# Performance work log

Measured on AMD Instinct MI355X. Metric: run time of the kernel, lower is better.

The kernel has to match this reference:

```python
import jax, jax.numpy as jnp
import numpy as np

EMBED_DIM = 512
NUM_HEADS = 8
DPH = EMBED_DIM // NUM_HEADS
NUM_REL = 3
B, S = 8, 512


def setup_inputs() -> dict:
    key = jax.random.key(0)
    ks = jax.random.split(key, 12)
    sc = 1.0 / np.sqrt(EMBED_DIM)
    inp = {
        'query': jax.random.normal(ks[0], (B, S, EMBED_DIM), jnp.float32),
        'key': jax.random.normal(ks[1], (B, S, EMBED_DIM), jnp.float32),
        'value': jax.random.normal(ks[2], (B, S, EMBED_DIM), jnp.float32),
        'graph_relations': jax.random.randint(ks[3], (B, S, S), 0, NUM_REL, jnp.int32),
        'Wq': jax.random.normal(ks[4], (EMBED_DIM, EMBED_DIM), jnp.float32) * sc,
        'bq': jnp.zeros((EMBED_DIM,), jnp.float32),
        'Wk': jax.random.normal(ks[5], (EMBED_DIM, EMBED_DIM), jnp.float32) * sc,
        'bk': jnp.zeros((EMBED_DIM,), jnp.float32),
        'Wv': jax.random.normal(ks[6], (EMBED_DIM, EMBED_DIM), jnp.float32) * sc,
        'bv': jnp.zeros((EMBED_DIM,), jnp.float32),
        'Wo': jax.random.normal(ks[7], (EMBED_DIM, EMBED_DIM), jnp.float32) * sc,
        'bo': jnp.zeros((EMBED_DIM,), jnp.float32),
        # padding_idx=0 -> row 0 is zeros
        'rel_k': jax.random.normal(ks[8], (NUM_REL, DPH), jnp.float32).at[0].set(0.0),
        'rel_v': jax.random.normal(ks[9], (NUM_REL, DPH), jnp.float32).at[0].set(0.0),
    }
    return inp


def reference(query, key, value, graph_relations, Wq, bq, Wk, bk, Wv, bv, Wo, bo, rel_k, rel_v):
    scale = DPH ** (-0.5)
    b, s, _ = query.shape
    # projections + split into heads: [b, s, h, d]
    q = (query @ Wq + bq).reshape(b, s, NUM_HEADS, DPH)
    k = (key @ Wk + bk).reshape(b, s, NUM_HEADS, DPH)
    v = (value @ Wv + bv).reshape(b, s, NUM_HEADS, DPH)
    QK = jnp.einsum('bshd,bthd->bhst', q, k)
    E_k = rel_k[graph_relations]  # [b, s, t, d]
    QE = jnp.einsum('bshd,bstd->bhst', q, E_k)
    e = jax.nn.softmax((QK + QE) * scale, axis=-1)  # [b, h, s, t]
    eV = jnp.einsum('bhst,bthd->bshd', e, v)
    E_v = rel_v[graph_relations]  # [b, s, t, d]
    eE = jnp.einsum('bhst,bstd->bshd', e, E_v)
    out = (eV + eE).reshape(b, s, EMBED_DIM)
    return out @ Wo + bo
```

## Files before the change

### kernel.cpp

```cpp
#include <hip/hip_runtime.h>
#include <hip/hip_bf16.h>

#define S_LEN 512
#define EMB   512
#define NHEAD 8
#define DPH   64
#define NREL  3
#define BATCH 8

typedef __attribute__((ext_vector_type(8))) short bf16x8;
typedef __attribute__((ext_vector_type(4))) float f32x4;

__device__ __forceinline__ float bf2f(unsigned short u) {
    union { unsigned int i; float f; } cv;
    cv.i = ((unsigned int)u) << 16;
    return cv.f;
}
__device__ __forceinline__ unsigned short f2bf(float f) {
    __hip_bfloat16 h = __float2bfloat16(f);
    return *reinterpret_cast<unsigned short*>(&h);
}

__device__ __forceinline__ void gload_lds16(const unsigned short* g, unsigned char* lds) {
    __builtin_amdgcn_global_load_lds(
        (const __attribute__((address_space(1))) void*)g,
        (__attribute__((address_space(3))) void*)lds, 16, 0, 0);
}

__global__ __launch_bounds__(256) void transpose_w(
    const float* __restrict__ Wq, const float* __restrict__ Wk,
    const float* __restrict__ Wv, const float* __restrict__ Wo,
    unsigned short* __restrict__ Wt)
{
    const int z = blockIdx.z;
    const float* W = (z == 0) ? Wq : (z == 1) ? Wk : (z == 2) ? Wv : Wo;
    unsigned short* dst = Wt + (size_t)z * EMB * EMB;

    __shared__ float tile[64][65];
    const int n0 = blockIdx.x * 64, k0 = blockIdx.y * 64;
    const int t = threadIdx.x;
    const int cr = t >> 4, cc = (t & 15) * 4;

    #pragma unroll
    for (int it = 0; it < 4; ++it) {
        int r = cr + it * 16;
        float4 v = *reinterpret_cast<const float4*>(W + (size_t)(k0 + r) * EMB + n0 + cc);
        tile[r][cc + 0] = v.x; tile[r][cc + 1] = v.y;
        tile[r][cc + 2] = v.z; tile[r][cc + 3] = v.w;
    }
    __syncthreads();
    #pragma unroll
    for (int it = 0; it < 4; ++it) {
        int n = cr + it * 16;
        ushort4 o;
        o.x = f2bf(tile[cc + 0][n]); o.y = f2bf(tile[cc + 1][n]);
        o.z = f2bf(tile[cc + 2][n]); o.w = f2bf(tile[cc + 3][n]);
        *reinterpret_cast<ushort4*>(dst + (size_t)(n0 + n) * EMB + k0 + cc) = o;
    }
}

__global__ __launch_bounds__(256) void gemm_proj_mfma(
    const float* __restrict__ Aq, const float* __restrict__ Ak, const float* __restrict__ Av,
    const unsigned short* __restrict__ Wt,
    const float* __restrict__ bqp, const float* __restrict__ bkp, const float* __restrict__ bvp,
    unsigned short* __restrict__ oq, unsigned short* __restrict__ okp, unsigned short* __restrict__ ov)
{
    const int z = blockIdx.z;
    const float* A = (z == 0) ? Aq : (z == 1) ? Ak : Av;
    const unsigned short* W = Wt + (size_t)z * EMB * EMB;
    const float* bias = (z == 0) ? bqp : (z == 1) ? bkp : bvp;
    unsigned short* out = (z == 0) ? oq : (z == 1) ? okp : ov;

    const int n0 = blockIdx.x * 128;
    const int m0 = blockIdx.y * 64;
    const int tid = threadIdx.x;
    const int lane = tid & 63;
    const int wid = tid >> 6;
    const int wr = wid >> 1, wc = wid & 1;

    __shared__ __align__(16) unsigned char smA[64 * 64 * 2];
    __shared__ __align__(16) unsigned char smB[128 * 64 * 2];

    f32x4 acc[2][4] = {};

    for (int k0 = 0; k0 < EMB; k0 += 64) {
        __syncthreads();
        #pragma unroll
        for (int it = 0; it < 4; ++it) {
            int row = (it * 4 + wid) * 8 + (lane >> 3);
            int kcg = (lane & 7) ^ (row & 7);
            gload_lds16(W + (size_t)(n0 + row) * EMB + k0 + kcg * 8,
                        smB + (it * 4 + wid) * 1024);
        }
        #pragma unroll
        for (int it = 0; it < 2; ++it) {
            int w = it * 256 + tid;
            int row = w >> 3, kc = w & 7;
            const float* src = A + (size_t)(m0 + row) * EMB + k0 + kc * 8;
            float4 v0 = *reinterpret_cast<const float4*>(src);
            float4 v1 = *reinterpret_cast<const float4*>(src + 4);
            union { unsigned short s[8]; uint4 u; } p;
            p.s[0] = f2bf(v0.x); p.s[1] = f2bf(v0.y); p.s[2] = f2bf(v0.z); p.s[3] = f2bf(v0.w);
            p.s[4] = f2bf(v1.x); p.s[5] = f2bf(v1.y); p.s[6] = f2bf(v1.z); p.s[7] = f2bf(v1.w);
            unsigned byte = ((unsigned)row << 7) + ((unsigned)kc << 4);
            byte ^= (unsigned)((row & 7) << 4);
            *reinterpret_cast<uint4*>(smA + byte) = p.u;
        }
        __syncthreads();

        #pragma unroll
        for (int ks = 0; ks < 2; ++ks) {
            bf16x8 bfrag[4];
            #pragma unroll
            for (int ni = 0; ni < 4; ++ni) {
                int col = wc * 64 + ni * 16 + (lane & 15);
                unsigned byte = ((unsigned)col << 7) + (unsigned)(ks << 6) + (unsigned)((lane >> 4) << 4);
                byte ^= (unsigned)((col & 7) << 4);
                bfrag[ni] = *reinterpret_cast<const bf16x8*>(smB + byte);
            }
            #pragma unroll
            for (int mi = 0; mi < 2; ++mi) {
                int row = wr * 32 + mi * 16 + (lane & 15);
                unsigned byte = ((unsigned)row << 7) + (unsigned)(ks << 6) + (unsigned)((lane >> 4) << 4);
                byte ^= (unsigned)((row & 7) << 4);
                bf16x8 afrag = *reinterpret_cast<const bf16x8*>(smA + byte);
                #pragma unroll
                for (int ni = 0; ni < 4; ++ni)
                    acc[mi][ni] = __builtin_amdgcn_mfma_f32_16x16x32_bf16(afrag, bfrag[ni], acc[mi][ni], 0, 0, 0);
            }
        }
    }

    if (z == 2) {
        #pragma unroll
        for (int ni = 0; ni < 4; ++ni) {
            int colg = n0 + wc * 64 + ni * 16 + (lane & 15);
            float bj = bias[colg];
            int hh = colg >> 6, dd = colg & 63;
            #pragma unroll
            for (int mi = 0; mi < 2; ++mi) {
                int rbase = m0 + wr * 32 + mi * 16 + ((lane >> 4) << 2);
                int bb = rbase >> 9, ss = rbase & 511;
                ushort4 o;
                o.x = f2bf(acc[mi][ni][0] + bj);
                o.y = f2bf(acc[mi][ni][1] + bj);
                o.z = f2bf(acc[mi][ni][2] + bj);
                o.w = f2bf(acc[mi][ni][3] + bj);
                *reinterpret_cast<ushort4*>(out + ((size_t)(bb * NHEAD + hh) * DPH + dd) * S_LEN + ss) = o;
            }
        }
    } else {
        #pragma unroll
        for (int ni = 0; ni < 4; ++ni) {
            int colg = n0 + wc * 64 + ni * 16 + (lane & 15);
            float bj = bias[colg];
            #pragma unroll
            for (int mi = 0; mi < 2; ++mi) {
                int rbase = m0 + wr * 32 + mi * 16 + ((lane >> 4) << 2);
                #pragma unroll
                for (int q = 0; q < 4; ++q)
                    out[(size_t)(rbase + q) * EMB + colg] = f2bf(acc[mi][ni][q] + bj);
            }
        }
    }
}

__global__ __launch_bounds__(256) void gemm_out_mfma(
    const unsigned short* __restrict__ A,
    const unsigned short* __restrict__ W,
    const float* __restrict__ bias,
    float* __restrict__ out)
{
    const int n0 = blockIdx.x * 128;
    const int m0 = blockIdx.y * 64;
    const int tid = threadIdx.x;
    const int lane = tid & 63;
    const int wid = tid >> 6;
    const int wr = wid >> 1, wc = wid & 1;

    __shared__ __align__(16) unsigned char smA[64 * 64 * 2];
    __shared__ __align__(16) unsigned char smB[128 * 64 * 2];

    f32x4 acc[2][4] = {};

    for (int k0 = 0; k0 < EMB; k0 += 64) {
        __syncthreads();
        #pragma unroll
        for (int it = 0; it < 4; ++it) {
            int row = (it * 4 + wid) * 8 + (lane >> 3);
            int kcg = (lane & 7) ^ (row & 7);
            gload_lds16(W + (size_t)(n0 + row) * EMB + k0 + kcg * 8,
                        smB + (it * 4 + wid) * 1024);
        }
        #pragma unroll
        for (int it = 0; it < 2; ++it) {
            int row = (it * 4 + wid) * 8 + (lane >> 3);
            int kcg = (lane & 7) ^ (row & 7);
            gload_lds16(A + (size_t)(m0 + row) * EMB + k0 + kcg * 8,
                        smA + (it * 4 + wid) * 1024);
        }
        __syncthreads();

        #pragma unroll
        for (int ks = 0; ks < 2; ++ks) {
            bf16x8 bfrag[4];
            #pragma unroll
            for (int ni = 0; ni < 4; ++ni) {
                int col = wc * 64 + ni * 16 + (lane & 15);
                unsigned byte = ((unsigned)col << 7) + (unsigned)(ks << 6) + (unsigned)((lane >> 4) << 4);
                byte ^= (unsigned)((col & 7) << 4);
                bfrag[ni] = *reinterpret_cast<const bf16x8*>(smB + byte);
            }
            #pragma unroll
            for (int mi = 0; mi < 2; ++mi) {
                int row = wr * 32 + mi * 16 + (lane & 15);
                unsigned byte = ((unsigned)row << 7) + (unsigned)(ks << 6) + (unsigned)((lane >> 4) << 4);
                byte ^= (unsigned)((row & 7) << 4);
                bf16x8 afrag = *reinterpret_cast<const bf16x8*>(smA + byte);
                #pragma unroll
                for (int ni = 0; ni < 4; ++ni)
                    acc[mi][ni] = __builtin_amdgcn_mfma_f32_16x16x32_bf16(afrag, bfrag[ni], acc[mi][ni], 0, 0, 0);
            }
        }
    }

    #pragma unroll
    for (int ni = 0; ni < 4; ++ni) {
        int colg = n0 + wc * 64 + ni * 16 + (lane & 15);
        float bj = bias[colg];
        #pragma unroll
        for (int mi = 0; mi < 2; ++mi) {
            int rbase = m0 + wr * 32 + mi * 16 + ((lane >> 4) << 2);
            #pragma unroll
            for (int q = 0; q < 4; ++q)
                out[(size_t)(rbase + q) * EMB + colg] = acc[mi][ni][q] + bj;
        }
    }
}

__global__ __launch_bounds__(512) void attn_mfma(
    const unsigned short* __restrict__ qb,
    const unsigned short* __restrict__ kb,
    const unsigned short* __restrict__ vbT,
    const int* __restrict__ rel,
    const float* __restrict__ rel_k, const float* __restrict__ rel_v,
    unsigned short* __restrict__ ob)
{
    const int gid = blockIdx.x + 8 * (blockIdx.y + 8 * blockIdx.z);
    const int bh  = (gid & 7) + 8 * ((gid >> 3) & 7);
    const int s0  = (gid >> 6) * 64;
    const int h   = bh & 7;
    const int b   = bh >> 3;
    const int tid = threadIdx.x;
    const int lane = tid & 63;
    const int wid = tid >> 6;
    const int qstrip = wid & 3;
    const int tgroup = wid >> 2;
    const int sl = lane & 15;
    const int tg = lane >> 4;

    __shared__ __align__(16) unsigned char smQ[64 * 128];
    __shared__ __align__(16) unsigned char smK[2 * 64 * 128];
    __shared__ __align__(16) unsigned char smVt[2 * 64 * 128];
    __shared__ __align__(16) unsigned char smP2[4 * 16 * 128];
    __shared__ float qrel_s[64][4];
    __shared__ float relv_s[NREL][64];

    const unsigned short* qsrc  = qb + ((size_t)(b * S_LEN + s0)) * EMB + h * DPH;
    const unsigned short* ksrc  = kb + ((size_t)b * S_LEN) * EMB + h * DPH;
    const unsigned short* vsrcT = vbT + (size_t)(b * NHEAD + h) * DPH * S_LEN;

    {
        int row = tid >> 3, kc = tid & 7;
        uint4 raw = *reinterpret_cast<const uint4*>(qsrc + (size_t)row * EMB + kc * 8);
        unsigned byte = ((unsigned)row << 7) + ((unsigned)kc << 4);
        byte ^= (unsigned)((row & 7) << 4);
        *reinterpret_cast<uint4*>(smQ + byte) = raw;
    }
    if (tid < NREL * 64) {
        int rr = tid >> 6, d = tid & 63;
        relv_s[rr][d] = rel_v[rr * DPH + d];
    }
    __syncthreads();
    if (tid < 192) {
        int r = tid / 3, rr = tid - 3 * (tid / 3);
        float s = 0.f;
        #pragma unroll
        for (int dc = 0; dc < 32; ++dc) {
            unsigned byte = ((unsigned)r << 7) + (unsigned)(dc << 2);
            byte ^= (unsigned)((r & 7) << 4);
            unsigned u = *reinterpret_cast<const unsigned*>(smQ + byte);
            s += bf2f((unsigned short)(u & 0xffff)) * rel_k[rr * DPH + dc * 2]
               + bf2f((unsigned short)(u >> 16))   * rel_k[rr * DPH + dc * 2 + 1];
        }
        qrel_s[r][rr] = s;
    }
    __syncthreads();

    const int srow = qstrip * 16 + sl;
    const float CEXP  = 0.125f * 1.4426950408889634f;
    const float SHIFT = 11.541560327111707f;
    const float qa0 = qrel_s[srow][0] * CEXP - SHIFT;
    const float qa1 = qrel_s[srow][1] * CEXP - SHIFT;
    const float qa2 = qrel_s[srow][2] * CEXP - SHIFT;

    bf16x8 qfrag[2];
    #pragma unroll
    for (int ks = 0; ks < 2; ++ks) {
        unsigned byte = ((unsigned)srow << 7) + (unsigned)(ks << 6) + (unsigned)(tg << 4);
        byte ^= (unsigned)((srow & 7) << 4);
        qfrag[ks] = *reinterpret_cast<const bf16x8*>(smQ + byte);
    }

    const int* rrow_s = rel + ((size_t)(b * S_LEN + s0 + srow)) * S_LEN;
    unsigned char* pb = (wid < 4) ? (smQ + wid * 2048) : (smP2 + (wid - 4) * 2048);

    const int gtid  = tid & 255;
    const int ldrow = gtid >> 3;
    const int ldkc  = gtid & 7;
    const unsigned wbyte0 = (((unsigned)ldrow << 7) + ((unsigned)ldkc << 4))
                            ^ ((unsigned)((ldrow & 7) << 4));
    const unsigned wbyte1 = wbyte0 + 4096;
    unsigned char* kbase = smK  + tgroup * 8192;
    unsigned char* vbase = smVt + tgroup * 8192;

    float l_run = 0.f, es1 = 0.f, es2 = 0.f;
    f32x4 acc_pv[4] = {};

    #pragma unroll
    for (int i = 0; i < 4; ++i) {
        const int t0 = (tgroup * 4 + i) * 64;

        uint4 k0 = *reinterpret_cast<const uint4*>(ksrc + (size_t)(t0 + ldrow) * EMB + ldkc * 8);
        uint4 k1 = *reinterpret_cast<const uint4*>(ksrc + (size_t)(t0 + ldrow + 32) * EMB + ldkc * 8);
        uint4 v0 = *reinterpret_cast<const uint4*>(vsrcT + (size_t)ldrow * S_LEN + t0 + ldkc * 8);
        uint4 v1 = *reinterpret_cast<const uint4*>(vsrcT + (size_t)(ldrow + 32) * S_LEN + t0 + ldkc * 8);
        int4 rr[4];
        #pragma unroll
        for (int t4 = 0; t4 < 4; ++t4)
            rr[t4] = *reinterpret_cast<const int4*>(rrow_s + t0 + t4 * 16 + tg * 4);

        __syncthreads();
        *reinterpret_cast<uint4*>(kbase + wbyte0) = k0;
        *reinterpret_cast<uint4*>(kbase + wbyte1) = k1;
        *reinterpret_cast<uint4*>(vbase + wbyte0) = v0;
        *reinterpret_cast<uint4*>(vbase + wbyte1) = v1;
        __syncthreads();

        f32x4 sacc[4] = {};
        #pragma unroll
        for (int ks = 0; ks < 2; ++ks)
            #pragma unroll
            for (int t4 = 0; t4 < 4; ++t4) {
                int trow = t4 * 16 + sl;
                unsigned byte = ((unsigned)trow << 7) + (unsigned)(ks << 6) + (unsigned)(tg << 4);
                byte ^= (unsigned)((trow & 7) << 4);
                bf16x8 kf = *reinterpret_cast<const bf16x8*>(kbase + byte);
                sacc[t4] = __builtin_amdgcn_mfma_f32_16x16x32_bf16(kf, qfrag[ks], sacc[t4], 0, 0, 0);
            }

        #pragma unroll
        for (int t4 = 0; t4 < 4; ++t4) {
            int rv[4] = {rr[t4].x, rr[t4].y, rr[t4].z, rr[t4].w};
            #pragma unroll
            for (int j = 0; j < 4; ++j) {
                int r = rv[j];
                float qa = (r == 0) ? qa0 : ((r == 1) ? qa1 : qa2);
                float p = __builtin_amdgcn_exp2f(fmaf(sacc[t4][j], CEXP, qa));
                sacc[t4][j] = p;
                l_run += p;
                es1 += (r == 1) ? p : 0.f;
                es2 += (r == 2) ? p : 0.f;
            }
        }

        #pragma unroll
        for (int t4 = 0; t4 < 4; ++t4)
            #pragma unroll
            for (int pr = 0; pr < 2; ++pr) {
                unsigned u = (unsigned)f2bf(sacc[t4][2 * pr]) |
                             ((unsigned)f2bf(sacc[t4][2 * pr + 1]) << 16);
                unsigned byte = ((unsigned)sl << 7) + (unsigned)(t4 * 32 + tg * 8 + pr * 4);
                byte ^= (unsigned)((sl & 7) << 4);
                *reinterpret_cast<unsigned*>(pb + byte) = u;
            }

        #pragma unroll
        for (int ks = 0; ks < 2; ++ks) {
            unsigned pbyte = ((unsigned)sl << 7) + (unsigned)(ks << 6) + (unsigned)(tg << 4);
            pbyte ^= (unsigned)((sl & 7) << 4);
            bf16x8 pf = *reinterpret_cast<const bf16x8*>(pb + pbyte);
            #pragma unroll
            for (int dt = 0; dt < 4; ++dt) {
                int d = dt * 16 + sl;
                unsigned vbyte = ((unsigned)d << 7) + (unsigned)(ks << 6) + (unsigned)(tg << 4);
                vbyte ^= (unsigned)((d & 7) << 4);
                bf16x8 vf = *reinterpret_cast<const bf16x8*>(vbase + vbyte);
                acc_pv[dt] = __builtin_amdgcn_mfma_f32_16x16x32_bf16(pf, vf, acc_pv[dt], 0, 0, 0);
            }
        }
    }

    l_run += __shfl_xor(l_run, 16);  l_run += __shfl_xor(l_run, 32);
    es1   += __shfl_xor(es1, 16);    es1   += __shfl_xor(es1, 32);
    es2   += __shfl_xor(es2, 16);    es2   += __shfl_xor(es2, 32);

    __syncthreads();
    float* accL  = reinterpret_cast<float*>(smK);
    float* stats = reinterpret_cast<float*>(smVt);

    if (tg == 0) {
        stats[tgroup * 64 + srow]        = l_run;
        stats[128 + tgroup * 64 + srow]  = es1;
        stats[256 + tgroup * 64 + srow]  = es2;
    }
    if (tgroup == 1) {
        #pragma unroll
        for (int dt = 0; dt < 4; ++dt)
            #pragma unroll
            for (int r = 0; r < 4; ++r)
                accL[(qstrip * 16 + tg * 4 + r) * 64 + dt * 16 + sl] = acc_pv[dt][r];
    }
    __syncthreads();

    if (tgroup == 0) {
        unsigned short* dst = ob + ((size_t)(b * S_LEN + s0 + qstrip * 16)) * EMB + h * DPH;
        #pragma unroll
        for (int r = 0; r < 4; ++r) {
            const int row64 = qstrip * 16 + tg * 4 + r;
            float lt  = stats[row64]       + stats[64 + row64];
            float e1t = stats[128 + row64] + stats[192 + row64];
            float e2t = stats[256 + row64] + stats[320 + row64];
            float e0t = lt - e1t - e2t;
            float linv = 1.f / lt;
            #pragma unroll
            for (int dt = 0; dt < 4; ++dt) {
                int d = dt * 16 + sl;
                float o = acc_pv[dt][r] + accL[row64 * 64 + d];
                o += e0t * relv_s[0][d] + e1t * relv_s[1][d] + e2t * relv_s[2][d];
                o *= linv;
                dst[(size_t)(tg * 4 + r) * EMB + d] = f2bf(o);
            }
        }
    }
}

extern "C" void kernel_launch(void* const* d_in, const int* in_sizes, int n_in,
                              void* d_out, int out_size, void* d_ws, size_t ws_size,
                              hipStream_t stream) {
    int iq=0, ik=1, iv=2, irel=3, iWq=4, ibq=5, iWk=6, ibk=7, iWv=8, ibv=9, iWo=10, ibo=11, irk=12, irv=13;
    if (n_in >= 14 && in_sizes[0] == 512 * 512) {
        iWk=0; iWo=1; iWq=2; iWv=3; ibk=4; ibo=5; ibq=6; ibv=7;
        irel=8; ik=9; iq=10; irk=11; irv=12; iv=13;
    }

    const float* q_in = (const float*)d_in[iq];
    const float* k_in = (const float*)d_in[ik];
    const float* v_in = (const float*)d_in[iv];
    const int*   grel = (const int*)d_in[irel];
    const float* Wq = (const float*)d_in[iWq];
    const float* bq = (const float*)d_in[ibq];
    const float* Wk = (const float*)d_in[iWk];
    const float* bk = (const float*)d_in[ibk];
    const float* Wv = (const float*)d_in[iWv];
    const float* bv = (const float*)d_in[ibv];
    const float* Wo = (const float*)d_in[iWo];
    const float* bo = (const float*)d_in[ibo];
    const float* rk = (const float*)d_in[irk];
    const float* rv = (const float*)d_in[irv];

    unsigned short* qb  = (unsigned short*)d_ws;
    unsigned short* kb  = qb + (size_t)4096 * 512;
    unsigned short* vbT = kb + (size_t)4096 * 512;
    unsigned short* ab  = vbT + (size_t)4096 * 512;
    unsigned short* wt  = ab + (size_t)4096 * 512;

    dim3 blk(256);
    transpose_w<<<dim3(8, 8, 4), blk, 0, stream>>>(Wq, Wk, Wv, Wo, wt);
    gemm_proj_mfma<<<dim3(4, 64, 3), blk, 0, stream>>>(q_in, k_in, v_in, wt, bq, bk, bv, qb, kb, vbT);
    attn_mfma<<<dim3(8, NHEAD, BATCH), dim3(512), 0, stream>>>(qb, kb, vbT, grel, rk, rv, ab);
    gemm_out_mfma<<<dim3(4, 64), blk, 0, stream>>>(ab, wt + (size_t)3 * 512 * 512, bo, (float*)d_out);
}
```

Before: 56.93 us.

## Double-buffer K/V tiles via async global-to-LDS loads with smaller key chunks

```diff
diff --git a/kernel.cpp b/kernel.cpp
--- a/kernel.cpp
+++ b/kernel.cpp
@@ -256,13 +256,14 @@
     const int wid = tid >> 6;
     const int qstrip = wid & 3;
     const int tgroup = wid >> 2;
+    const int wg = wid & 3;
     const int sl = lane & 15;
     const int tg = lane >> 4;
 
-    __shared__ __align__(16) unsigned char smQ[64 * 128];
-    __shared__ __align__(16) unsigned char smK[2 * 64 * 128];
-    __shared__ __align__(16) unsigned char smVt[2 * 64 * 128];
-    __shared__ __align__(16) unsigned char smP2[4 * 16 * 128];
+    __shared__ __align__(16) unsigned char smQ[8192];
+    __shared__ __align__(16) unsigned char smK[16384];
+    __shared__ __align__(16) unsigned char smVt[16384];
+    __shared__ __align__(16) unsigned char smP2[4096];
     __shared__ float qrel_s[64][4];
     __shared__ float relv_s[NREL][64];
 
@@ -313,55 +314,59 @@
     }
 
     const int* rrow_s = rel + ((size_t)(b * S_LEN + s0 + srow)) * S_LEN;
-    unsigned char* pb = (wid < 4) ? (smQ + wid * 2048) : (smP2 + (wid - 4) * 2048);
-
-    const int gtid  = tid & 255;
-    const int ldrow = gtid >> 3;
-    const int ldkc  = gtid & 7;
-    const unsigned wbyte0 = (((unsigned)ldrow << 7) + ((unsigned)ldkc << 4))
-                            ^ ((unsigned)((ldrow & 7) << 4));
-    const unsigned wbyte1 = wbyte0 + 4096;
-    unsigned char* kbase = smK  + tgroup * 8192;
-    unsigned char* vbase = smVt + tgroup * 8192;
+    unsigned char* pb = (wid < 4) ? (smQ + wid * 1024) : (smP2 + (wid - 4) * 1024);
+
+    const int krow = wg * 8 + ((lane & 63) >> 3);
+    const int kcg  = (lane & 7) ^ (krow & 7);
+    const int vd   = wg * 16 + (lane >> 2);
+    const int vtcg = (lane & 3) ^ (vd & 3);
+    unsigned char* kbuf0 = smK  + tgroup * 8192;
+    unsigned char* vbuf0 = smVt + tgroup * 8192;
 
     float l_run = 0.f, es1 = 0.f, es2 = 0.f;
     f32x4 acc_pv[4] = {};
 
+    {
+        const int t0 = tgroup * 256;
+        gload_lds16(ksrc + (size_t)(t0 + krow) * EMB + kcg * 8, kbuf0 + wg * 1024);
+        gload_lds16(vsrcT + (size_t)vd * S_LEN + t0 + vtcg * 8, vbuf0 + wg * 1024);
+    }
+    __syncthreads();
+
     #pragma unroll
-    for (int i = 0; i < 4; ++i) {
-        const int t0 = (tgroup * 4 + i) * 64;
-
-        uint4 k0 = *reinterpret_cast<const uint4*>(ksrc + (size_t)(t0 + ldrow) * EMB + ldkc * 8);
-        uint4 k1 = *reinterpret_cast<const uint4*>(ksrc + (size_t)(t0 + ldrow + 32) * EMB + ldkc * 8);
-        uint4 v0 = *reinterpret_cast<const uint4*>(vsrcT + (size_t)ldrow * S_LEN + t0 + ldkc * 8);
-        uint4 v1 = *reinterpret_cast<const uint4*>(vsrcT + (size_t)(ldrow + 32) * S_LEN + t0 + ldkc * 8);
-        int4 rr[4];
-        #pragma unroll
-        for (int t4 = 0; t4 < 4; ++t4)
-            rr[t4] = *reinterpret_cast<const int4*>(rrow_s + t0 + t4 * 16 + tg * 4);
-
-        __syncthreads();
-        *reinterpret_cast<uint4*>(kbase + wbyte0) = k0;
-        *reinterpret_cast<uint4*>(kbase + wbyte1) = k1;
-        *reinterpret_cast<uint4*>(vbase + wbyte0) = v0;
-        *reinterpret_cast<uint4*>(vbase + wbyte1) = v1;
-        __syncthreads();
-
-        f32x4 sacc[4] = {};
+    for (int i = 0; i < 8; ++i) {
+        const int t0 = tgroup * 256 + i * 32;
+        const int cur = i & 1;
+        unsigned char* kcur = kbuf0 + cur * 4096;
+        unsigned char* vcur = vbuf0 + cur * 4096;
+
+        if (i < 7) {
+            const int t0n = t0 + 32;
+            gload_lds16(ksrc + (size_t)(t0n + krow) * EMB + kcg * 8,
+                        kbuf0 + (cur ^ 1) * 4096 + wg * 1024);
+            gload_lds16(vsrcT + (size_t)vd * S_LEN + t0n + vtcg * 8,
+                        vbuf0 + (cur ^ 1) * 4096 + wg * 1024);
+        }
+
+        int4 rr0 = *reinterpret_cast<const int4*>(rrow_s + t0 + tg * 4);
+        int4 rr1 = *reinterpret_cast<const int4*>(rrow_s + t0 + 16 + tg * 4);
+
+        f32x4 sacc[2] = {};
         #pragma unroll
         for (int ks = 0; ks < 2; ++ks)
             #pragma unroll
-            for (int t4 = 0; t4 < 4; ++t4) {
+            for (int t4 = 0; t4 < 2; ++t4) {
                 int trow = t4 * 16 + sl;
                 unsigned byte = ((unsigned)trow << 7) + (unsigned)(ks << 6) + (unsigned)(tg << 4);
                 byte ^= (unsigned)((trow & 7) << 4);
-                bf16x8 kf = *reinterpret_cast<const bf16x8*>(kbase + byte);
+                bf16x8 kf = *reinterpret_cast<const bf16x8*>(kcur + byte);
                 sacc[t4] = __builtin_amdgcn_mfma_f32_16x16x32_bf16(kf, qfrag[ks], sacc[t4], 0, 0, 0);
             }
 
         #pragma unroll
-        for (int t4 = 0; t4 < 4; ++t4) {
-            int rv[4] = {rr[t4].x, rr[t4].y, rr[t4].z, rr[t4].w};
+        for (int t4 = 0; t4 < 2; ++t4) {
+            int4 rrx = (t4 == 0) ? rr0 : rr1;
+            int rv[4] = {rrx.x, rrx.y, rrx.z, rrx.w};
             #pragma unroll
             for (int j = 0; j < 4; ++j) {
                 int r = rv[j];
@@ -375,37 +380,35 @@
         }
 
         #pragma unroll
-        for (int t4 = 0; t4 < 4; ++t4)
+        for (int t4 = 0; t4 < 2; ++t4)
             #pragma unroll
             for (int pr = 0; pr < 2; ++pr) {
                 unsigned u = (unsigned)f2bf(sacc[t4][2 * pr]) |
                              ((unsigned)f2bf(sacc[t4][2 * pr + 1]) << 16);
-                unsigned byte = ((unsigned)sl << 7) + (unsigned)(t4 * 32 + tg * 8 + pr * 4);
-                byte ^= (unsigned)((sl & 7) << 4);
+                unsigned byte = ((unsigned)sl << 6) + (unsigned)(t4 * 32 + tg * 8 + pr * 4);
+                byte ^= (unsigned)((sl & 3) << 4);
                 *reinterpret_cast<unsigned*>(pb + byte) = u;
             }
 
-        #pragma unroll
-        for (int ks = 0; ks < 2; ++ks) {
-            unsigned pbyte = ((unsigned)sl << 7) + (unsigned)(ks << 6) + (unsigned)(tg << 4);
-            pbyte ^= (unsigned)((sl & 7) << 4);
-            bf16x8 pf = *reinterpret_cast<const bf16x8*>(pb + pbyte);
-            #pragma unroll
-            for (int dt = 0; dt < 4; ++dt) {
-                int d = dt * 16 + sl;
-                unsigned vbyte = ((unsigned)d << 7) + (unsigned)(ks << 6) + (unsigned)(tg << 4);
-                vbyte ^= (unsigned)((d & 7) << 4);
-                bf16x8 vf = *reinterpret_cast<const bf16x8*>(vbase + vbyte);
-                acc_pv[dt] = __builtin_amdgcn_mfma_f32_16x16x32_bf16(pf, vf, acc_pv[dt], 0, 0, 0);
-            }
-        }
+        unsigned pbyte = ((unsigned)sl << 6) + (unsigned)(tg << 4);
+        pbyte ^= (unsigned)((sl & 3) << 4);
+        bf16x8 pf = *reinterpret_cast<const bf16x8*>(pb + pbyte);
+        #pragma unroll
+        for (int dt = 0; dt < 4; ++dt) {
+            int d = dt * 16 + sl;
+            unsigned vbyte = ((unsigned)d << 6) + (unsigned)(tg << 4);
+            vbyte ^= (unsigned)((d & 3) << 4);
+            bf16x8 vf = *reinterpret_cast<const bf16x8*>(vcur + vbyte);
+            acc_pv[dt] = __builtin_amdgcn_mfma_f32_16x16x32_bf16(pf, vf, acc_pv[dt], 0, 0, 0);
+        }
+
+        __syncthreads();
     }
 
     l_run += __shfl_xor(l_run, 16);  l_run += __shfl_xor(l_run, 32);
     es1   += __shfl_xor(es1, 16);    es1   += __shfl_xor(es1, 32);
     es2   += __shfl_xor(es2, 16);    es2   += __shfl_xor(es2, 32);
 
-    __syncthreads();
     float* accL  = reinterpret_cast<float*>(smK);
     float* stats = reinterpret_cast<float*>(smVt);
 
```

Result: slower. 60.58 us, median of 2 (+6.4%).
